# Performance work log

Hardware: AMD Instinct MI355X
Metric: run time of the kernel (lower is better)

The kernel has to match this reference:

```python
import jax, jax.numpy as jnp
import numpy as np

N_HEADS = 16

def setup_inputs() -> dict:
    key = jax.random.key(0)
    ks = jax.random.split(key, 5)
    B, N, D = 2, 2048, 1024
    return {
        "x": jax.random.normal(ks[0], (B, N, D), dtype=jnp.float32),
        "w_qkv": jax.random.normal(ks[1], (D, 3 * D), dtype=jnp.float32) * (1.0 / np.sqrt(D)),
        "b_qkv": jax.random.normal(ks[2], (3 * D,), dtype=jnp.float32) * 0.02,
        "w_out": jax.random.normal(ks[3], (D, D), dtype=jnp.float32) * (1.0 / np.sqrt(D)),
        "b_out": jax.random.normal(ks[4], (D,), dtype=jnp.float32) * 0.02,
    }

def reference(x, w_qkv, b_qkv, w_out, b_out):
    B, N, D = x.shape
    H = N_HEADS
    dk = D // H
    qkv = x @ w_qkv + b_qkv                       # (B, N, 3D)
    # NOTE: original reshapes to (B, N, H, 3*dk) then chunks -> per-head interleaved layout
    qkv = qkv.reshape(B, N, H, 3 * dk).transpose(2, 0, 1, 3)  # (H, B, N, 3*dk)
    q, k, v = jnp.split(qkv, 3, axis=-1)          # each (H, B, N, dk)
    scale = 1.0 / np.sqrt(dk).astype(np.float32)
    scores = jnp.einsum('hbnd,hbmd->hbnm', q, k) * scale  # (H, B, N, N)
    attn = jax.nn.softmax(scores, axis=-1)
    context = jnp.einsum('hbnm,hbmd->hbnd', attn, v)       # (H, B, N, dk)
    context = context.transpose(1, 2, 0, 3).reshape(B, N, D)
    attn_mean = attn.mean(axis=0).mean(axis=1)    # (B, N): mean over heads then over query dim
    out = context @ w_out + b_out
    return out, attn_mean
```

## Files before the change

### kernel.cpp

```cpp
#include <hip/hip_runtime.h>
#include <hip/hip_bf16.h>
#include <stdint.h>

#define B_ 2
#define N_ 2048
#define D_ 1024
#define H_ 16
#define DK 64

typedef __bf16 bf16x8 __attribute__((ext_vector_type(8)));
typedef short s16x4 __attribute__((ext_vector_type(4)));
typedef float f32x4 __attribute__((ext_vector_type(4)));

#define EXP2SC 0.18033688011112042f

__device__ __forceinline__ unsigned short f2bf(float f) {
    unsigned int u = __float_as_uint(f);
    u = (u + 0x7FFFu + ((u >> 16) & 1u)) >> 16;
    return (unsigned short)u;
}

__device__ __forceinline__ short2 pkbf(float a, float b) {
    __hip_bfloat162 t = __float22bfloat162_rn(float2{a, b});
    return *(short2*)&t;
}

__device__ __forceinline__ void glds16(const void* g, void* l) {
    __builtin_amdgcn_global_load_lds(
        (const __attribute__((address_space(1))) void*)g,
        (__attribute__((address_space(3))) void*)l, 16, 0, 0);
}

__global__ __launch_bounds__(256) void k_prep(const float* __restrict__ x,
                                              unsigned short* __restrict__ xb,
                                              const float* __restrict__ w_qkv,
                                              unsigned short* __restrict__ wqkvT,
                                              const float* __restrict__ w_out,
                                              unsigned short* __restrict__ woutT,
                                              float* __restrict__ amean) {
    __shared__ float tile[32][33];
    int blk = blockIdx.x, t = threadIdx.x;
    if (blk < 1024) {
        const float4* x4 = (const float4*)x;
        ushort4* o4 = (ushort4*)xb;
        int i = blk * 256 + t;
#pragma unroll
        for (int s = 0; s < 4; ++s, i += 262144) {
            float4 v = x4[i];
            ushort4 o;
            o.x = f2bf(v.x); o.y = f2bf(v.y); o.z = f2bf(v.z); o.w = f2bf(v.w);
            o4[i] = o;
        }
    } else if (blk < 4096) {
        int idx = blk - 1024;
        int c0 = (idx % 96) * 32, k0 = (idx / 96) * 32;
        int tx = t & 31, ty = t >> 5;
        for (int s = 0; s < 4; ++s)
            tile[ty + 8 * s][tx] = w_qkv[(size_t)(k0 + ty + 8 * s) * 3072 + c0 + tx];
        __syncthreads();
        for (int s = 0; s < 4; ++s)
            wqkvT[(size_t)(c0 + ty + 8 * s) * 1024 + k0 + tx] = f2bf(tile[tx][ty + 8 * s]);
    } else if (blk < 5120) {
        int idx = blk - 4096;
        int c0 = (idx % 32) * 32, k0 = (idx / 32) * 32;
        int tx = t & 31, ty = t >> 5;
        for (int s = 0; s < 4; ++s)
            tile[ty + 8 * s][tx] = w_out[(size_t)(k0 + ty + 8 * s) * 1024 + c0 + tx];
        __syncthreads();
        for (int s = 0; s < 4; ++s)
            woutT[(size_t)(c0 + ty + 8 * s) * 1024 + k0 + tx] = f2bf(tile[tx][ty + 8 * s]);
    } else {
#pragma unroll
        for (int s = 0; s < 16; ++s) amean[s * 256 + t] = 0.f;
    }
}

__global__ __launch_bounds__(256) void k_gemm_qkv(const unsigned short* __restrict__ A,
                                                  const unsigned short* __restrict__ BT,
                                                  const float* __restrict__ bias,
                                                  unsigned short* __restrict__ Cout,
                                                  int M, int Nn, int K) {
    __shared__ __attribute__((aligned(16))) unsigned short lds[32768];
    int t = threadIdx.x;
    int lane = t & 63, w = t >> 6;
    int quad = lane >> 4, c = lane & 15;
    int wm = w >> 1, wn = w & 1;
    int bi = blockIdx.y, bj = blockIdx.x;
    const unsigned short* Abase = A + (size_t)(bi * 128) * K;
    const unsigned short* Bbase = BT + (size_t)(bj * 128) * K;

    f32x4 acc[4][4];
#pragma unroll
    for (int mf = 0; mf < 4; ++mf)
#pragma unroll
        for (int nf = 0; nf < 4; ++nf)
            acc[mf][nf] = (f32x4){0.f, 0.f, 0.f, 0.f};

    auto stage = [&](int k0, int p) {
        unsigned short* Ab = lds + p * 16384;
        unsigned short* Bb = Ab + 8192;
#pragma unroll
        for (int i = 0; i < 4; ++i) {
            int ch = i * 256 + t;
            int row = ch >> 3, kc = (ch & 7) ^ (row & 7);
            glds16(&Abase[(size_t)row * K + k0 + kc * 8], (char*)Ab + ch * 16);
            glds16(&Bbase[(size_t)row * K + k0 + kc * 8], (char*)Bb + ch * 16);
        }
    };
    stage(0, 0);

    for (int kb = 0; kb < 16; ++kb) {
        __syncthreads();
        if (kb < 15) stage((kb + 1) * 64, (kb + 1) & 1);
        const unsigned short* Ab = lds + (kb & 1) * 16384;
        const unsigned short* Bb = Ab + 8192;
#pragma unroll
        for (int ks = 0; ks < 2; ++ks) {
            bf16x8 af[4], bfr[4];
#pragma unroll
            for (int mf = 0; mf < 4; ++mf)
                af[mf] = *(const bf16x8*)&Ab[(wm * 64 + mf * 16 + c) * 64 +
                                             (((ks * 4 + quad) ^ (c & 7)) * 8)];
#pragma unroll
            for (int nf = 0; nf < 4; ++nf)
                bfr[nf] = *(const bf16x8*)&Bb[(wn * 64 + nf * 16 + c) * 64 +
                                              (((ks * 4 + quad) ^ (c & 7)) * 8)];
#pragma unroll
            for (int mf = 0; mf < 4; ++mf)
#pragma unroll
                for (int nf = 0; nf < 4; ++nf)
                    acc[mf][nf] = __builtin_amdgcn_mfma_f32_16x16x32_bf16(af[mf], bfr[nf],
                                                                          acc[mf][nf], 0, 0, 0);
        }
    }

#pragma unroll
    for (int mf = 0; mf < 4; ++mf)
#pragma unroll
        for (int nf = 0; nf < 4; ++nf) {
            int j = bj * 128 + wn * 64 + nf * 16 + c;
            float bv = bias[j];
            int h = j / 192, r2 = j % 192;
            int which = r2 >> 6, d = r2 & 63;
#pragma unroll
            for (int r = 0; r < 4; ++r) {
                int i = bi * 128 + wm * 64 + mf * 16 + quad * 4 + r;
                float v = acc[mf][nf][r] + bv;
                if (which == 0) v *= EXP2SC;
                int b = i >> 11, n = i & 2047;
                size_t dst;
                if (which < 2)
                    dst = (size_t)which * 4194304 + (((size_t)(h * 2 + b) * 2048 + n) * 64 + d);
                else
                    dst = (size_t)2 * 4194304 + (((size_t)(h * 2 + b) * 64 + d) * 2048 + n);
                Cout[dst] = f2bf(v);
            }
        }
}

__global__ __launch_bounds__(256) void k_gemm_out(const unsigned short* __restrict__ A,
                                                  const unsigned short* __restrict__ BT,
                                                  const float* __restrict__ bias,
                                                  float* __restrict__ C,
                                                  int M, int Nn, int K) {
    __shared__ __attribute__((aligned(16))) unsigned short lds[24576];
    int t = threadIdx.x;
    int lane = t & 63, w = t >> 6;
    int quad = lane >> 4, c = lane & 15;
    int wm = w >> 1, wn = w & 1;
    int bi = blockIdx.y, bj = blockIdx.x;
    const unsigned short* Abase = A + (size_t)(bi * 64) * K;
    const unsigned short* Bbase = BT + (size_t)(bj * 128) * K;

    f32x4 acc[2][4];
#pragma unroll
    for (int mf = 0; mf < 2; ++mf)
#pragma unroll
        for (int nf = 0; nf < 4; ++nf)
            acc[mf][nf] = (f32x4){0.f, 0.f, 0.f, 0.f};

    auto stage = [&](int k0, int p) {
        unsigned short* Ab = lds + p * 12288;
        unsigned short* Bb = Ab + 4096;
#pragma unroll
        for (int i = 0; i < 2; ++i) {
            int ch = i * 256 + t;
            int row = ch >> 3, kc = (ch & 7) ^ (row & 7);
            glds16(&Abase[(size_t)row * K + k0 + kc * 8], (char*)Ab + ch * 16);
        }
#pragma unroll
        for (int i = 0; i < 4; ++i) {
            int ch = i * 256 + t;
            int row = ch >> 3, kc = (ch & 7) ^ (row & 7);
            glds16(&Bbase[(size_t)row * K + k0 + kc * 8], (char*)Bb + ch * 16);
        }
    };
    stage(0, 0);

    for (int kb = 0; kb < 16; ++kb) {
        __syncthreads();
        if (kb < 15) stage((kb + 1) * 64, (kb + 1) & 1);
        const unsigned short* Ab = lds + (kb & 1) * 12288;
        const unsigned short* Bb = Ab + 4096;
#pragma unroll
        for (int ks = 0; ks < 2; ++ks) {
            bf16x8 af[2], bfr[4];
#pragma unroll
            for (int mf = 0; mf < 2; ++mf)
                af[mf] = *(const bf16x8*)&Ab[(wm * 32 + mf * 16 + c) * 64 +
                                             (((ks * 4 + quad) ^ (c & 7)) * 8)];
#pragma unroll
            for (int nf = 0; nf < 4; ++nf)
                bfr[nf] = *(const bf16x8*)&Bb[(wn * 64 + nf * 16 + c) * 64 +
                                              (((ks * 4 + quad) ^ (c & 7)) * 8)];
#pragma unroll
            for (int mf = 0; mf < 2; ++mf)
#pragma unroll
                for (int nf = 0; nf < 4; ++nf)
                    acc[mf][nf] = __builtin_amdgcn_mfma_f32_16x16x32_bf16(af[mf], bfr[nf],
                                                                          acc[mf][nf], 0, 0, 0);
        }
    }

#pragma unroll
    for (int mf = 0; mf < 2; ++mf)
#pragma unroll
        for (int nf = 0; nf < 4; ++nf) {
            int j = bj * 128 + wn * 64 + nf * 16 + c;
            float bv = bias[j];
#pragma unroll
            for (int r = 0; r < 4; ++r) {
                int i = bi * 64 + wm * 32 + mf * 16 + quad * 4 + r;
                C[(size_t)i * Nn + j] = acc[mf][nf][r] + bv;
            }
        }
}

__global__ __launch_bounds__(512) void k_attn(const unsigned short* __restrict__ Q,
                                              const unsigned short* __restrict__ Kc,
                                              const unsigned short* __restrict__ VT,
                                              unsigned short* __restrict__ ctx,
                                              float* __restrict__ lrs_out) {
    __shared__ __attribute__((aligned(16))) unsigned short lds[16384];
    int t = threadIdx.x, lane = t & 63, w = t >> 6;
    int quad = lane >> 4, c = lane & 15;
    int bi = blockIdx.x;
    int hb = bi & 31, qt = bi >> 5;
    int h = hb >> 1, b = hb & 1;
    const unsigned short* qbase = Q + (size_t)hb * 131072 + (size_t)(qt * 256 + w * 32) * 64;
    const unsigned short* kbase = Kc + (size_t)hb * 131072;
    const unsigned short* vtbase = VT + (size_t)hb * 131072;

    int srow = t >> 3, sB = t & 7;
    int sgoff = srow * 64 + ((sB ^ (srow & 7)) * 8);
    int vgoff = srow * 2048 + ((sB ^ (srow & 7)) * 8);

    bf16x8 qf[2][2];
#pragma unroll
    for (int qs = 0; qs < 2; ++qs)
#pragma unroll
        for (int ks = 0; ks < 2; ++ks)
            qf[qs][ks] = *(const bf16x8*)&qbase[(qs * 16 + c) * 64 + ks * 32 + quad * 8];

    glds16(&kbase[sgoff], (char*)lds + t * 16);
    glds16(&vtbase[vgoff], (char*)(lds + 4096) + t * 16);

    f32x4 acc[2][4];
#pragma unroll
    for (int qs = 0; qs < 2; ++qs)
#pragma unroll
        for (int ds = 0; ds < 4; ++ds) acc[qs][ds] = (f32x4){0.f, 0.f, 0.f, 0.f};
    float lsum[2] = {0.f, 0.f};

    for (int kb = 0; kb < 32; ++kb) {
        const unsigned short* Kb = lds + (kb & 1) * 8192;
        const unsigned short* Vb = Kb + 4096;
        __syncthreads();
        if (kb < 31) {
            unsigned short* Kn = lds + ((kb + 1) & 1) * 8192;
            glds16(&kbase[(size_t)(kb + 1) * 4096 + sgoff], (char*)Kn + t * 16);
            glds16(&vtbase[(size_t)(kb + 1) * 64 + vgoff], (char*)(Kn + 4096) + t * 16);
        }

        f32x4 st[4][2];
#pragma unroll
        for (int ksub = 0; ksub < 4; ++ksub)
#pragma unroll
            for (int qs = 0; qs < 2; ++qs) st[ksub][qs] = (f32x4){0.f, 0.f, 0.f, 0.f};
#pragma unroll
        for (int ks = 0; ks < 2; ++ks)
#pragma unroll
            for (int ksub = 0; ksub < 4; ++ksub) {
                bf16x8 kf = *(const bf16x8*)&Kb[(ksub * 16 + c) * 64 +
                                                (((ks * 4 + quad) ^ (c & 7)) * 8)];
#pragma unroll
                for (int qs = 0; qs < 2; ++qs)
                    st[ksub][qs] =
                        __builtin_amdgcn_mfma_f32_16x16x32_bf16(kf, qf[qs][ks], st[ksub][qs],
                                                                0, 0, 0);
            }
#pragma unroll
        for (int ksub = 0; ksub < 4; ++ksub) {
            s16x4 pf[2];
#pragma unroll
            for (int qs = 0; qs < 2; ++qs) {
                float p0 = __builtin_amdgcn_exp2f(st[ksub][qs][0]);
                float p1 = __builtin_amdgcn_exp2f(st[ksub][qs][1]);
                float p2 = __builtin_amdgcn_exp2f(st[ksub][qs][2]);
                float p3 = __builtin_amdgcn_exp2f(st[ksub][qs][3]);
                lsum[qs] += (p0 + p1) + (p2 + p3);
                short2 lo = pkbf(p0, p1), hi = pkbf(p2, p3);
                pf[qs] = (s16x4){lo.x, lo.y, hi.x, hi.y};
            }
            s16x4 vf[4];
#pragma unroll
            for (int ds = 0; ds < 4; ++ds) {
                int row = ds * 16 + c;
                vf[ds] = *(const s16x4*)&Vb[row * 64 +
                                            (((2 * ksub + (quad >> 1)) ^ (row & 7)) * 8) +
                                            (quad & 1) * 4];
            }
#pragma unroll
            for (int qs = 0; qs < 2; ++qs)
#pragma unroll
                for (int ds = 0; ds < 4; ++ds)
                    acc[qs][ds] = __builtin_amdgcn_mfma_f32_16x16x16bf16_1k(pf[qs], vf[ds],
                                                                            acc[qs][ds], 0, 0, 0);
        }
    }

#pragma unroll
    for (int qs = 0; qs < 2; ++qs) {
        float v = lsum[qs];
        v += __shfl_xor(v, 16);
        v += __shfl_xor(v, 32);
        if (lane < 16)
            lrs_out[hb * 2048 + qt * 256 + w * 32 + qs * 16 + c] =
                -(__builtin_amdgcn_logf(v) + 15.0f);
        float linv = 1.0f / v;
        float ir[4];
#pragma unroll
        for (int r = 0; r < 4; ++r) ir[r] = __shfl(linv, quad * 4 + r);
#pragma unroll
        for (int ds = 0; ds < 4; ++ds)
#pragma unroll
            for (int r = 0; r < 4; ++r) {
                int n = qt * 256 + w * 32 + qs * 16 + quad * 4 + r;
                ctx[((size_t)(b * 2048 + n)) * 1024 + h * 64 + ds * 16 + c] =
                    f2bf(acc[qs][ds][r] * ir[r]);
            }
    }
}

__global__ __launch_bounds__(512) void k_amean(const unsigned short* __restrict__ Q,
                                               const unsigned short* __restrict__ Kc,
                                               const float* __restrict__ lrs,
                                               float* __restrict__ amean) {
    __shared__ __attribute__((aligned(16))) unsigned short Qlds[16384];
    __shared__ float rslds[2][128];
    int t = threadIdx.x, lane = t & 63, w = t >> 6;
    int quad = lane >> 4, c = lane & 15;
    int bi = blockIdx.x;
    int hb = bi & 31, kt = bi >> 5, b = hb & 1;
    const unsigned short* kbase = Kc + (size_t)hb * 131072 + (size_t)(kt * 256 + w * 32) * 64;
    const unsigned short* qbase = Q + (size_t)hb * 131072;

    bf16x8 kf[2][2];
#pragma unroll
    for (int ksub = 0; ksub < 2; ++ksub)
#pragma unroll
        for (int ks = 0; ks < 2; ++ks)
            kf[ksub][ks] = *(const bf16x8*)&kbase[(ksub * 16 + c) * 64 + ks * 32 + quad * 8];

#pragma unroll
    for (int i = 0; i < 2; ++i) {
        int ch = i * 512 + t;
        int row = ch >> 3, Bs = ch & 7;
        glds16(&qbase[row * 64 + ((Bs ^ (row & 7)) * 8)], (char*)Qlds + ch * 16);
    }
    if (t < 128) rslds[0][t] = lrs[hb * 2048 + t];

    f32x4 colacc[2];
    colacc[0] = (f32x4){0.f, 0.f, 0.f, 0.f};
    colacc[1] = (f32x4){0.f, 0.f, 0.f, 0.f};

    for (int qc = 0; qc < 16; ++qc) {
        const unsigned short* Qb = Qlds + (qc & 1) * 8192;
        __syncthreads();
        if (qc < 15) {
            unsigned short* Qn = Qlds + ((qc + 1) & 1) * 8192;
#pragma unroll
            for (int i = 0; i < 2; ++i) {
                int ch = i * 512 + t;
                int row = ch >> 3, Bs = ch & 7;
                glds16(&qbase[(size_t)(qc + 1) * 8192 + row * 64 + ((Bs ^ (row & 7)) * 8)],
                       (char*)Qn + ch * 16);
            }
            if (t < 128) rslds[(qc + 1) & 1][t] = lrs[hb * 2048 + (qc + 1) * 128 + t];
        }
#pragma unroll
        for (int qs = 0; qs < 8; ++qs) {
            f32x4 st[2];
            st[0] = (f32x4){0.f, 0.f, 0.f, 0.f};
            st[1] = (f32x4){0.f, 0.f, 0.f, 0.f};
#pragma unroll
            for (int ks = 0; ks < 2; ++ks) {
                bf16x8 qfr = *(const bf16x8*)&Qb[(qs * 16 + c) * 64 +
                                                 (((ks * 4 + quad) ^ (c & 7)) * 8)];
#pragma unroll
                for (int ksub = 0; ksub < 2; ++ksub)
                    st[ksub] = __builtin_amdgcn_mfma_f32_16x16x32_bf16(kf[ksub][ks], qfr,
                                                                       st[ksub], 0, 0, 0);
            }
            float rv = rslds[qc & 1][qs * 16 + c];
#pragma unroll
            for (int ksub = 0; ksub < 2; ++ksub)
#pragma unroll
                for (int r = 0; r < 4; ++r)
                    colacc[ksub][r] += __builtin_amdgcn_exp2f(st[ksub][r] + rv);
        }
    }
#pragma unroll
    for (int ksub = 0; ksub < 2; ++ksub)
#pragma unroll
        for (int r = 0; r < 4; ++r) {
            float v = colacc[ksub][r];
            v += __shfl_xor(v, 1);
            v += __shfl_xor(v, 2);
            v += __shfl_xor(v, 4);
            v += __shfl_xor(v, 8);
            if (c == 0)
                atomicAdd(&amean[b * 2048 + kt * 256 + w * 32 + ksub * 16 + quad * 4 + r], v);
        }
}

extern "C" void kernel_launch(void* const* d_in, const int* in_sizes, int n_in,
                              void* d_out, int out_size, void* d_ws, size_t ws_size,
                              hipStream_t stream) {
    const float* x = (const float*)d_in[0];
    const float* w_qkv = (const float*)d_in[1];
    const float* b_qkv = (const float*)d_in[2];
    const float* w_out = (const float*)d_in[3];
    const float* b_out = (const float*)d_in[4];
    float* out = (float*)d_out;
    float* amean = out + 4194304;

    unsigned short* ws = (unsigned short*)d_ws;
    unsigned short* x_bf = ws;
    unsigned short* wqkvT = x_bf + 4194304;
    unsigned short* woutT = wqkvT + 3145728;
    unsigned short* q_bf = woutT + 1048576;
    unsigned short* k_bf = q_bf + 4194304;
    unsigned short* vT_bf = k_bf + 4194304;
    unsigned short* ctx_bf = vT_bf + 4194304;
    float* lrs = (float*)(ctx_bf + 4194304);

    k_prep<<<5121, 256, 0, stream>>>(x, x_bf, w_qkv, wqkvT, w_out, woutT, amean);
    k_gemm_qkv<<<dim3(24, 32), 256, 0, stream>>>(x_bf, wqkvT, b_qkv, q_bf, 4096, 3072, 1024);
    k_attn<<<256, 512, 0, stream>>>(q_bf, k_bf, vT_bf, ctx_bf, lrs);
    k_amean<<<256, 512, 0, stream>>>(q_bf, k_bf, lrs, amean);
    k_gemm_out<<<dim3(8, 64), 256, 0, stream>>>(ctx_bf, woutT, b_out, out, 4096, 1024, 1024);
}
```

Before: 208.8 us.

## Split attention and attn-mean kernels along key/query halves with combine pass

The attention kernel now splits the key dimension into two halves, launching twice as many blocks, and writes unnormalized fp16 partial outputs and partial row sums. A new combine kernel adds the halves, normalizes, and writes the bf16 context and log row sums. The attention-mean kernel is likewise split across query halves to double its grid. This aims to raise occupancy and CU utilization, at the cost of extra partial-result memory traffic, an extra launch, and fp16 precision on the partials.

After: 217.2 us. 1.04x slower.

```diff
diff --git a/kernel.cpp b/kernel.cpp
--- a/kernel.cpp
+++ b/kernel.cpp
@@ -11,6 +11,7 @@
 typedef __bf16 bf16x8 __attribute__((ext_vector_type(8)));
 typedef short s16x4 __attribute__((ext_vector_type(4)));
 typedef float f32x4 __attribute__((ext_vector_type(4)));
+typedef _Float16 f16x4v __attribute__((ext_vector_type(4)));
 
 #define EXP2SC 0.18033688011112042f
 
@@ -239,17 +240,17 @@
 __global__ __launch_bounds__(512) void k_attn(const unsigned short* __restrict__ Q,
                                               const unsigned short* __restrict__ Kc,
                                               const unsigned short* __restrict__ VT,
-                                              unsigned short* __restrict__ ctx,
-                                              float* __restrict__ lrs_out) {
+                                              _Float16* __restrict__ Opart,
+                                              float* __restrict__ lpart) {
     __shared__ __attribute__((aligned(16))) unsigned short lds[16384];
     int t = threadIdx.x, lane = t & 63, w = t >> 6;
     int quad = lane >> 4, c = lane & 15;
     int bi = blockIdx.x;
-    int hb = bi & 31, qt = bi >> 5;
-    int h = hb >> 1, b = hb & 1;
+    int hb = bi & 31, rest = bi >> 5;
+    int qt = rest >> 1, kh = rest & 1;
     const unsigned short* qbase = Q + (size_t)hb * 131072 + (size_t)(qt * 256 + w * 32) * 64;
-    const unsigned short* kbase = Kc + (size_t)hb * 131072;
-    const unsigned short* vtbase = VT + (size_t)hb * 131072;
+    const unsigned short* kbase = Kc + (size_t)hb * 131072 + (size_t)kh * 65536;
+    const unsigned short* vtbase = VT + (size_t)hb * 131072 + (size_t)kh * 1024;
 
     int srow = t >> 3, sB = t & 7;
     int sgoff = srow * 64 + ((sB ^ (srow & 7)) * 8);
@@ -272,11 +273,11 @@
         for (int ds = 0; ds < 4; ++ds) acc[qs][ds] = (f32x4){0.f, 0.f, 0.f, 0.f};
     float lsum[2] = {0.f, 0.f};
 
-    for (int kb = 0; kb < 32; ++kb) {
+    for (int kb = 0; kb < 16; ++kb) {
         const unsigned short* Kb = lds + (kb & 1) * 8192;
         const unsigned short* Vb = Kb + 4096;
         __syncthreads();
-        if (kb < 31) {
+        if (kb < 15) {
             unsigned short* Kn = lds + ((kb + 1) & 1) * 8192;
             glds16(&kbase[(size_t)(kb + 1) * 4096 + sgoff], (char*)Kn + t * 16);
             glds16(&vtbase[(size_t)(kb + 1) * 64 + vgoff], (char*)(Kn + 4096) + t * 16);
@@ -334,22 +335,39 @@
         float v = lsum[qs];
         v += __shfl_xor(v, 16);
         v += __shfl_xor(v, 32);
+        int nbase = qt * 256 + w * 32 + qs * 16;
         if (lane < 16)
-            lrs_out[hb * 2048 + qt * 256 + w * 32 + qs * 16 + c] =
-                -(__builtin_amdgcn_logf(v) + 15.0f);
-        float linv = 1.0f / v;
-        float ir[4];
-#pragma unroll
-        for (int r = 0; r < 4; ++r) ir[r] = __shfl(linv, quad * 4 + r);
+            lpart[kh * 65536 + hb * 2048 + nbase + c] = v;
 #pragma unroll
         for (int ds = 0; ds < 4; ++ds)
 #pragma unroll
             for (int r = 0; r < 4; ++r) {
-                int n = qt * 256 + w * 32 + qs * 16 + quad * 4 + r;
-                ctx[((size_t)(b * 2048 + n)) * 1024 + h * 64 + ds * 16 + c] =
-                    f2bf(acc[qs][ds][r] * ir[r]);
-            }
-    }
+                size_t row = (size_t)hb * 2048 + nbase + quad * 4 + r;
+                Opart[(row * 2 + kh) * 64 + ds * 16 + c] =
+                    (_Float16)(acc[qs][ds][r] * 0.0009765625f);
+            }
+    }
+}
+
+__global__ __launch_bounds__(256) void k_combine(const _Float16* __restrict__ Opart,
+                                                 const float* __restrict__ lpart,
+                                                 unsigned short* __restrict__ ctx,
+                                                 float* __restrict__ lrs) {
+    int g = blockIdx.x * 256 + threadIdx.x;
+    int row = g >> 4, q4 = g & 15;
+    int hb = row >> 11, n = row & 2047;
+    int h = hb >> 1, b = hb & 1;
+    float l = lpart[row] + lpart[65536 + row];
+    float s = 1024.0f / l;
+    if (q4 == 0) lrs[row] = -(__builtin_amdgcn_logf(l) + 15.0f);
+    f16x4v a = *(const f16x4v*)&Opart[((size_t)row * 2) * 64 + q4 * 4];
+    f16x4v d = *(const f16x4v*)&Opart[((size_t)row * 2 + 1) * 64 + q4 * 4];
+    ushort4 o;
+    o.x = f2bf(((float)a[0] + (float)d[0]) * s);
+    o.y = f2bf(((float)a[1] + (float)d[1]) * s);
+    o.z = f2bf(((float)a[2] + (float)d[2]) * s);
+    o.w = f2bf(((float)a[3] + (float)d[3]) * s);
+    *(ushort4*)&ctx[((size_t)(b * 2048 + n)) * 1024 + h * 64 + q4 * 4] = o;
 }
 
 __global__ __launch_bounds__(512) void k_amean(const unsigned short* __restrict__ Q,
@@ -361,7 +379,9 @@
     int t = threadIdx.x, lane = t & 63, w = t >> 6;
     int quad = lane >> 4, c = lane & 15;
     int bi = blockIdx.x;
-    int hb = bi & 31, kt = bi >> 5, b = hb & 1;
+    int hb = bi & 31, rest = bi >> 5;
+    int kt = rest >> 1, qh = rest & 1, b = hb & 1;
+    int qc0 = qh * 8;
     const unsigned short* kbase = Kc + (size_t)hb * 131072 + (size_t)(kt * 256 + w * 32) * 64;
     const unsigned short* qbase = Q + (size_t)hb * 131072;
 
@@ -376,18 +396,19 @@
     for (int i = 0; i < 2; ++i) {
         int ch = i * 512 + t;
         int row = ch >> 3, Bs = ch & 7;
-        glds16(&qbase[row * 64 + ((Bs ^ (row & 7)) * 8)], (char*)Qlds + ch * 16);
-    }
-    if (t < 128) rslds[0][t] = lrs[hb * 2048 + t];
+        glds16(&qbase[(size_t)qc0 * 8192 + row * 64 + ((Bs ^ (row & 7)) * 8)],
+               (char*)Qlds + ch * 16);
+    }
+    if (t < 128) rslds[0][t] = lrs[hb * 2048 + qc0 * 128 + t];
 
     f32x4 colacc[2];
     colacc[0] = (f32x4){0.f, 0.f, 0.f, 0.f};
     colacc[1] = (f32x4){0.f, 0.f, 0.f, 0.f};
 
-    for (int qc = 0; qc < 16; ++qc) {
+    for (int qc = qc0; qc < qc0 + 8; ++qc) {
         const unsigned short* Qb = Qlds + (qc & 1) * 8192;
         __syncthreads();
-        if (qc < 15) {
+        if (qc < qc0 + 7) {
             unsigned short* Qn = Qlds + ((qc + 1) & 1) * 8192;
 #pragma unroll
             for (int i = 0; i < 2; ++i) {
@@ -454,10 +475,13 @@
     unsigned short* vT_bf = k_bf + 4194304;
     unsigned short* ctx_bf = vT_bf + 4194304;
     float* lrs = (float*)(ctx_bf + 4194304);
+    float* lpart = lrs + 65536;
+    _Float16* Opart = (_Float16*)(lpart + 131072);
 
     k_prep<<<5121, 256, 0, stream>>>(x, x_bf, w_qkv, wqkvT, w_out, woutT, amean);
     k_gemm_qkv<<<dim3(24, 32), 256, 0, stream>>>(x_bf, wqkvT, b_qkv, q_bf, 4096, 3072, 1024);
-    k_attn<<<256, 512, 0, stream>>>(q_bf, k_bf, vT_bf, ctx_bf, lrs);
-    k_amean<<<256, 512, 0, stream>>>(q_bf, k_bf, lrs, amean);
+    k_attn<<<512, 512, 0, stream>>>(q_bf, k_bf, vT_bf, Opart, lpart);
+    k_combine<<<4096, 256, 0, stream>>>(Opart, lpart, ctx_bf, lrs);
+    k_amean<<<512, 512, 0, stream>>>(q_bf, k_bf, lrs, amean);
     k_gemm_out<<<dim3(8, 64), 256, 0, stream>>>(ctx_bf, woutT, b_out, out, 4096, 1024, 1024);
 }
```
